# Performance work log

Measured on AMD Instinct MI355X. Metric: run time of the kernel, lower is better.

## Reference

```python
import jax, jax.numpy as jnp
import numpy as np

HEADS, DIM_HEAD = 8, 64
EPS = 1e-5  # torch InstanceNorm1d default


def instance_norm(t):
    # torch InstanceNorm1d(dim_head) applied to (b*h, n, d) normalizes over the
    # last dim d for each (b, h, n); affine=False, biased variance.
    mu = jnp.mean(t, axis=-1, keepdims=True)
    var = jnp.mean((t - mu) ** 2, axis=-1, keepdims=True)
    return (t - mu) * jax.lax.rsqrt(var + EPS)


def setup_inputs() -> dict:
    key = jax.random.key(0)
    k1, k2, k3, k4 = jax.random.split(key, 4)
    B, N, D = 8, 8192, 256
    inner = HEADS * DIM_HEAD  # 512
    x = jax.random.normal(k1, (B, N, D), jnp.float32)
    w_qkv = jax.random.normal(k2, (3 * inner, D), jnp.float32) / np.sqrt(D).astype(np.float32)
    w_out = jax.random.normal(k3, (D, inner), jnp.float32) / np.sqrt(inner).astype(np.float32)
    b_out = 0.01 * jax.random.normal(k4, (D,), jnp.float32)
    return {"x": x, "w_qkv": w_qkv, "w_out": w_out, "b_out": b_out}


def reference(x, w_qkv, w_out, b_out):
    B, N, _ = x.shape
    H, Dh = HEADS, DIM_HEAD
    # fused qkv projection: [B,N,3*H*Dh]
    qkv = jnp.einsum('bnd,ed->bne', x, w_qkv)
    q, k, v = jnp.split(qkv, 3, axis=-1)

    def to_heads(t):
        return t.reshape(B, N, H, Dh).transpose(0, 2, 1, 3)  # b h n d

    q, k, v = to_heads(q), to_heads(k), to_heads(v)
    # galerkin: instance-norm K and V
    k = instance_norm(k)
    v = instance_norm(v)
    # linear (non-softmax) attention: (K^T V) then Q @ (K^T V), scaled by 1/N
    dots = jnp.einsum('bhnd,bhne->bhde', k, v)            # [B,H,Dh,Dh]
    out = jnp.einsum('bhnd,bhde->bhne', q, dots) / N      # [B,H,N,Dh]
    out = out.transpose(0, 2, 1, 3).reshape(B, N, H * Dh)
    return jnp.einsum('bne,de->bnd', out, w_out) + b_out
```

## Files before the change

kernel.cpp:

```cpp
#include <hip/hip_runtime.h>
#include <hip/hip_bf16.h>
#include <stdint.h>

typedef __attribute__((ext_vector_type(8))) __bf16 bf16x8;
typedef __attribute__((ext_vector_type(8))) unsigned short ushort8_t;
typedef __attribute__((ext_vector_type(4))) unsigned short ushort4_t;
typedef __attribute__((ext_vector_type(4))) float f32x4;

#define MFMA16(a, b, c) __builtin_amdgcn_mfma_f32_16x16x32_bf16((a), (b), (c), 0, 0, 0)

static __device__ __forceinline__ unsigned short f2bf(float f) {
  union { float f; unsigned u; } v; v.f = f;
  unsigned r = v.u + 0x7fffu + ((v.u >> 16) & 1u);
  return (unsigned short)(r >> 16);
}
static __device__ __forceinline__ float bf2f(unsigned short u) {
  union { unsigned u; float f; } v; v.u = ((unsigned)u) << 16; return v.f;
}

static __device__ __forceinline__ void gld_lds16(const void* g, void* l) {
  __builtin_amdgcn_global_load_lds((const __attribute__((address_space(1))) void*)g,
                                   (__attribute__((address_space(3))) void*)l, 16, 0, 0);
}

__global__ __launch_bounds__(256) void k_conv(const float* __restrict__ x,
                                              const float* __restrict__ wqkv,
                                              const float* __restrict__ wout,
                                              unsigned short* __restrict__ xb,
                                              unsigned short* __restrict__ wqb,
                                              unsigned short* __restrict__ woutb) {
  const size_t NX = 4194304;
  const size_t NW = 98304;
  const size_t NO = 32768;
  const size_t stride = (size_t)gridDim.x * 256;
  for (size_t i4 = (size_t)blockIdx.x * 256 + threadIdx.x; i4 < NX + NW + NO; i4 += stride) {
    const float* src; unsigned short* dst; size_t off;
    if (i4 < NX)           { src = x;    dst = xb;    off = i4; }
    else if (i4 < NX + NW) { src = wqkv; dst = wqb;   off = i4 - NX; }
    else                   { src = wout; dst = woutb; off = i4 - NX - NW; }
    float4 v = ((const float4*)src)[off];
    ushort4_t o = { f2bf(v.x), f2bf(v.y), f2bf(v.z), f2bf(v.w) };
    *(ushort4_t*)(dst + off * 4) = o;
  }
}

__global__ __launch_bounds__(512) void k_fused(const unsigned short* __restrict__ xb,
                                               const unsigned short* __restrict__ wqb,
                                               float* __restrict__ partials) {
  __shared__ __align__(16) char smem[65536];
  unsigned short* As = (unsigned short*)smem;
  unsigned short* Bs = (unsigned short*)(smem + 32768);
  unsigned short* kt = (unsigned short*)smem;
  unsigned short* vt = (unsigned short*)(smem + 18432);

  const int t = threadIdx.x;
  const int w = t >> 6, lane = t & 63, lr = lane & 15, lg = lane >> 4;
  const int wr = w >> 1, wc = w & 1;
  const int dblk = w >> 1, ep = w & 1;

  const int id = blockIdx.x;
  const int nid = (id & 7) * 128 + (id >> 3);
  const int mg = nid >> 3, h = nid & 7;

  const int srl = lane >> 3, sc = lane & 7;
  const int swz = (sc ^ srl) << 3;

  const unsigned short* bptr[2];
  int aoff[2];
#pragma unroll
  for (int i = 0; i < 2; ++i) {
    const int br = (w * 2 + i) * 8 + srl;
    const int grow = (br < 64) ? (512 + h * 64 + br) : (1024 + h * 64 + (br - 64));
    bptr[i] = wqb + (size_t)grow * 256 + swz;
    aoff[i] = br * 256 + swz;
  }

  f32x4 acc2[2] = {f32x4{0.f, 0.f, 0.f, 0.f}, f32x4{0.f, 0.f, 0.f, 0.f}};

  for (int mi = 0; mi < 4; ++mi) {
    const long m0 = ((long)mg * 4 + mi) * 128;
    const unsigned short* am = xb + (size_t)m0 * 256;

#pragma unroll
    for (int i = 0; i < 2; ++i) {
      gld_lds16(am + aoff[i], &As[(w * 2 + i) * 512]);
      gld_lds16(bptr[i],      &Bs[(w * 2 + i) * 512]);
    }
    __syncthreads();

    f32x4 acc[2][4];
#pragma unroll
    for (int mb = 0; mb < 2; ++mb)
#pragma unroll
      for (int nb = 0; nb < 4; ++nb) acc[mb][nb] = f32x4{0.f, 0.f, 0.f, 0.f};

    for (int ktt = 0; ktt < 4; ++ktt) {
      const int cur = ktt & 1, nxt = cur ^ 1;
      if (ktt < 3) {
        const int k0 = (ktt + 1) * 64;
#pragma unroll
        for (int i = 0; i < 2; ++i) {
          gld_lds16(am + aoff[i] + k0, &As[nxt * 8192 + (w * 2 + i) * 512]);
          gld_lds16(bptr[i] + k0,      &Bs[nxt * 8192 + (w * 2 + i) * 512]);
        }
      }
      bf16x8 a[2][2], b[4][2];
#pragma unroll
      for (int mb = 0; mb < 2; ++mb) {
        const int R = wr * 32 + mb * 16 + lr;
#pragma unroll
        for (int kh = 0; kh < 2; ++kh)
          a[mb][kh] = *(const bf16x8*)&As[cur * 8192 + R * 64 + ((((kh << 2) + lg) ^ (R & 7)) << 3)];
      }
#pragma unroll
      for (int nb = 0; nb < 4; ++nb) {
        const int E = wc * 64 + nb * 16 + lr;
#pragma unroll
        for (int kh = 0; kh < 2; ++kh)
          b[nb][kh] = *(const bf16x8*)&Bs[cur * 8192 + E * 64 + ((((kh << 2) + lg) ^ (E & 7)) << 3)];
      }
#pragma unroll
      for (int mb = 0; mb < 2; ++mb)
#pragma unroll
        for (int nb = 0; nb < 4; ++nb)
#pragma unroll
          for (int kh = 0; kh < 2; ++kh)
            acc[mb][nb] = MFMA16(a[mb][kh], b[nb][kh], acc[mb][nb]);
      __syncthreads();
    }

    unsigned short* dst = (wc == 0) ? kt : vt;
#pragma unroll
    for (int mb = 0; mb < 2; ++mb) {
#pragma unroll
      for (int rg = 0; rg < 4; ++rg) {
        float s1 = acc[mb][0][rg] + acc[mb][1][rg] + acc[mb][2][rg] + acc[mb][3][rg];
        float s2 = acc[mb][0][rg] * acc[mb][0][rg] + acc[mb][1][rg] * acc[mb][1][rg] +
                   acc[mb][2][rg] * acc[mb][2][rg] + acc[mb][3][rg] * acc[mb][3][rg];
        s1 += __shfl_xor(s1, 1); s2 += __shfl_xor(s2, 1);
        s1 += __shfl_xor(s1, 2); s2 += __shfl_xor(s2, 2);
        s1 += __shfl_xor(s1, 4); s2 += __shfl_xor(s2, 4);
        s1 += __shfl_xor(s1, 8); s2 += __shfl_xor(s2, 8);
        const float mean = s1 * (1.f / 64.f);
        const float rs = rsqrtf(s2 * (1.f / 64.f) - mean * mean + 1e-5f);
        const int n = wr * 32 + mb * 16 + lg * 4 + rg;
        const int cn = n >> 6, nn = n & 63;
#pragma unroll
        for (int nb = 0; nb < 4; ++nb)
          dst[cn * 4608 + (nb * 16 + lr) * 72 + nn] = f2bf((acc[mb][nb][rg] - mean) * rs);
      }
    }
    __syncthreads();

#pragma unroll
    for (int cn = 0; cn < 2; ++cn) {
#pragma unroll
      for (int ns = 0; ns < 64; ns += 32) {
        bf16x8 af = *(const bf16x8*)&kt[cn * 4608 + (dblk * 16 + lr) * 72 + ns + lg * 8];
#pragma unroll
        for (int e = 0; e < 2; ++e) {
          bf16x8 bv = *(const bf16x8*)&vt[cn * 4608 + ((ep * 2 + e) * 16 + lr) * 72 + ns + lg * 8];
          acc2[e] = MFMA16(af, bv, acc2[e]);
        }
      }
    }
    __syncthreads();
  }

  float* pb = partials + ((size_t)mg * 8 + h) * 4096;
#pragma unroll
  for (int e = 0; e < 2; ++e)
#pragma unroll
    for (int rg = 0; rg < 4; ++rg) {
      const int d = dblk * 16 + lg * 4 + rg;
      const int eo = (ep * 2 + e) * 16 + lr;
      pb[d * 64 + eo] = acc2[e][rg];
    }
}

__global__ __launch_bounds__(256) void k_mmat(const float* __restrict__ partials,
                                              const float* __restrict__ wqkv,
                                              unsigned short* __restrict__ tmpT) {
  __shared__ float dl[4096];
  __shared__ float wqls[64 * 256];
  const int bh = blockIdx.x, b = bh >> 3, h = bh & 7;
  const int t = threadIdx.x;
#pragma unroll
  for (int i = 0; i < 4; ++i) {
    int off = t * 16 + i * 4;
    f32x4 s = {0.f, 0.f, 0.f, 0.f};
    for (int c = 0; c < 16; ++c) {
      const size_t chunk = (size_t)(b * 16 + c) * 8 + h;
      f32x4 p = *(const f32x4*)(partials + chunk * 4096 + off);
      s += p;
    }
    *(f32x4*)&dl[off] = s;
  }
#pragma unroll
  for (int i = 0; i < 16; ++i) {
    int idx4 = i * 256 + t;
    int d = idx4 >> 6, c4 = idx4 & 63;
    *(f32x4*)&wqls[d * 256 + c4 * 4] =
        *(const f32x4*)(wqkv + (size_t)(h * 64 + d) * 256 + c4 * 4);
  }
  __syncthreads();
  const int k = t;
  const float scale = 1.0f / 8192.0f;
  float res[64];
  for (int e = 0; e < 64; ++e) {
    float s = 0.f;
#pragma unroll
    for (int d = 0; d < 64; ++d) s += dl[d * 64 + e] * wqls[d * 256 + k];
    res[e] = s * scale;
  }
  unsigned short* dstp = tmpT + (size_t)b * 131072 + (size_t)k * 512 + h * 64;
#pragma unroll
  for (int e8 = 0; e8 < 8; ++e8) {
    ushort8_t o;
#pragma unroll
    for (int j = 0; j < 8; ++j) o[j] = f2bf(res[e8 * 8 + j]);
    *(ushort8_t*)(dstp + e8 * 8) = o;
  }
}

__global__ __launch_bounds__(256) void k_pmat(const unsigned short* __restrict__ woutb,
                                              const unsigned short* __restrict__ tmpT,
                                              unsigned short* __restrict__ pswz) {
  const int bid = blockIdx.x;
  const int b = bid >> 2, oq = (bid >> 1) & 1, kq = bid & 1;
  const int t = threadIdx.x, w = t >> 6, lane = t & 63, lr = lane & 15, lg = lane >> 4;
  const int wr = w >> 1, wc = w & 1;
  const int ob = oq * 128 + wr * 64, kb = kq * 128 + wc * 64;
  const unsigned short* tb = tmpT + (size_t)b * 131072;

  f32x4 acc[4][4];
#pragma unroll
  for (int mb = 0; mb < 4; ++mb)
#pragma unroll
    for (int nb = 0; nb < 4; ++nb) acc[mb][nb] = f32x4{0.f, 0.f, 0.f, 0.f};

  for (int ks = 0; ks < 16; ++ks) {
    bf16x8 a[4], bb[4];
#pragma unroll
    for (int mb = 0; mb < 4; ++mb)
      a[mb] = *(const bf16x8*)(woutb + (size_t)(ob + mb * 16 + lr) * 512 + ks * 32 + lg * 8);
#pragma unroll
    for (int nb = 0; nb < 4; ++nb)
      bb[nb] = *(const bf16x8*)(tb + (size_t)(kb + nb * 16 + lr) * 512 + ks * 32 + lg * 8);
#pragma unroll
    for (int mb = 0; mb < 4; ++mb)
#pragma unroll
      for (int nb = 0; nb < 4; ++nb) acc[mb][nb] = MFMA16(a[mb], bb[nb], acc[mb][nb]);
  }

  unsigned short* pb = pswz + (size_t)b * 65536;
#pragma unroll
  for (int mb = 0; mb < 4; ++mb)
#pragma unroll
    for (int nb = 0; nb < 4; ++nb)
#pragma unroll
      for (int rg = 0; rg < 4; ++rg) {
        int o = ob + mb * 16 + lg * 4 + rg;
        int k = kb + nb * 16 + lr;
        pb[(((k >> 5) * 16 + (o >> 4)) * 64 + (o & 15) + ((k >> 3) & 3) * 16) * 8 + (k & 7)] =
            f2bf(acc[mb][nb][rg]);
      }
}

__global__ __launch_bounds__(512) void k_gemm2(const unsigned short* __restrict__ xb,
                                               const unsigned short* __restrict__ pswz,
                                               const float* __restrict__ bout,
                                               float* __restrict__ out) {
  __shared__ __align__(16) char smem[65536];
  unsigned short* As = (unsigned short*)smem;
  float* lf = (float*)smem;

  const int b = blockIdx.x >> 6, mt = blockIdx.x & 63;
  const long m0 = (long)mt * 128;
  const int t = threadIdx.x, w = t >> 6, lane = t & 63, lr = lane & 15, lg = lane >> 4;
  const int wr = w >> 2, wc = w & 3;
  const unsigned short* qb = xb + ((size_t)b * 8192 + m0) * 256;
  const unsigned short* Mb = pswz + (size_t)b * 65536;
  const int srl = lane >> 3, sc = lane & 7;

#pragma unroll
  for (int i = 0; i < 2; ++i) {
    const int row = (i * 8 + w) * 8 + srl;
    gld_lds16(qb + (size_t)row * 256 + ((sc ^ (row & 7)) << 3),
              &As[(i * 8 + w) * 512]);
  }
  __syncthreads();

  f32x4 acc[4][4];
#pragma unroll
  for (int mb = 0; mb < 4; ++mb)
#pragma unroll
    for (int nb = 0; nb < 4; ++nb) acc[mb][nb] = f32x4{0.f, 0.f, 0.f, 0.f};

  for (int ks = 0; ks < 4; ++ks) {
    const int cur = ks & 1, nxt = cur ^ 1;
    if (ks < 3) {
      const int k0 = (ks + 1) * 64;
#pragma unroll
      for (int i = 0; i < 2; ++i) {
        const int row = (i * 8 + w) * 8 + srl;
        gld_lds16(qb + (size_t)row * 256 + k0 + ((sc ^ (row & 7)) << 3),
                  &As[nxt * 8192 + (i * 8 + w) * 512]);
      }
    }
    bf16x8 a[4][2], bfr[2][4];
#pragma unroll
    for (int mb = 0; mb < 4; ++mb) {
      const int R = wr * 64 + mb * 16 + lr;
#pragma unroll
      for (int kh = 0; kh < 2; ++kh)
        a[mb][kh] = *(const bf16x8*)&As[cur * 8192 + R * 64 + ((((kh << 2) + lg) ^ (R & 7)) << 3)];
    }
#pragma unroll
    for (int kh = 0; kh < 2; ++kh)
#pragma unroll
      for (int nb = 0; nb < 4; ++nb)
        bfr[kh][nb] = *(const bf16x8*)(Mb + ((((size_t)ks * 2 + kh) * 16 + wc * 4 + nb) * 64 + lane) * 8);
#pragma unroll
    for (int mb = 0; mb < 4; ++mb)
#pragma unroll
      for (int nb = 0; nb < 4; ++nb)
#pragma unroll
        for (int kh = 0; kh < 2; ++kh)
          acc[mb][nb] = MFMA16(a[mb][kh], bfr[kh][nb], acc[mb][nb]);
    __syncthreads();
  }

#pragma unroll
  for (int p = 0; p < 2; ++p) {
    if (wr == p) {
#pragma unroll
      for (int mb = 0; mb < 4; ++mb)
#pragma unroll
        for (int nb = 0; nb < 4; ++nb)
#pragma unroll
          for (int rg = 0; rg < 4; ++rg)
            lf[(mb * 16 + lg * 4 + rg) * 256 + wc * 64 + nb * 16 + lr] = acc[mb][nb][rg];
    }
    __syncthreads();
#pragma unroll
    for (int i = 0; i < 8; ++i) {
      const int idx = i * 512 + t;
      const int r = idx >> 6, c4 = idx & 63;
      f32x4 v = *(f32x4*)&lf[r * 256 + c4 * 4];
      f32x4 bo4 = *(const f32x4*)(bout + c4 * 4);
      v += bo4;
      *(f32x4*)(out + ((size_t)b * 8192 + m0 + p * 64 + r) * 256 + c4 * 4) = v;
    }
    __syncthreads();
  }
}

extern "C" void kernel_launch(void* const* d_in, const int* in_sizes, int n_in,
                              void* d_out, int out_size, void* d_ws, size_t ws_size,
                              hipStream_t stream) {
  const float* x    = (const float*)d_in[0];
  const float* wqkv = (const float*)d_in[1];
  const float* wout = (const float*)d_in[2];
  const float* bout = (const float*)d_in[3];
  float* out = (float*)d_out;

  char* ws = (char*)d_ws;
  unsigned short* xb = (unsigned short*)ws;
  size_t off = (size_t)65536 * 256 * 2;
  unsigned short* wqb = (unsigned short*)(ws + off);
  off += (size_t)1536 * 256 * 2;
  unsigned short* woutb = (unsigned short*)(ws + off);
  off += (size_t)256 * 512 * 2;
  float* partials = (float*)(ws + off);
  off += (size_t)1024 * 4096 * 4;
  unsigned short* tmpT = (unsigned short*)(ws + off);
  off += (size_t)8 * 131072 * 2;
  unsigned short* pswz = (unsigned short*)(ws + off);
  off += (size_t)8 * 65536 * 2;

  k_conv<<<4096, 256, 0, stream>>>(x, wqkv, wout, xb, wqb, woutb);
  k_fused<<<1024, 512, 0, stream>>>(xb, wqb, partials);
  k_mmat<<<64, 256, 0, stream>>>(partials, wqkv, tmpT);
  k_pmat<<<32, 256, 0, stream>>>(woutb, tmpT, pswz);
  k_gemm2<<<512, 512, 0, stream>>>(xb, pswz, bout, out);
}
```

Measured before the change: 164.4 us.

## Prefetch next M-tile during epilogue and relocate K/V scratch to avoid staging overlap

Moves the K/V normalized scratch buffers to the unused second halves of the A/B staging regions. This lets the first k-tile of the next M-tile be prefetched into buffer 0 during the last k-step and the normalization/KV-accumulation epilogue. Replaces some __syncthreads with LDS-only waitcnt plus barrier, drops the trailing barrier, switches the padded 72-stride scratch to an XOR-swizzled 64-stride layout, and fully unrolls the k loop. The goal is to hide global load latency across M-tiles, at the cost of subtler LDS hazard reasoning.

```diff
diff --git a/kernel.cpp b/kernel.cpp
--- a/kernel.cpp
+++ b/kernel.cpp
@@ -50,8 +50,8 @@
   __shared__ __align__(16) char smem[65536];
   unsigned short* As = (unsigned short*)smem;
   unsigned short* Bs = (unsigned short*)(smem + 32768);
-  unsigned short* kt = (unsigned short*)smem;
-  unsigned short* vt = (unsigned short*)(smem + 18432);
+  unsigned short* kt = (unsigned short*)smem + 8192;
+  unsigned short* vt = (unsigned short*)smem + 24576;
 
   const int t = threadIdx.x;
   const int w = t >> 6, lane = t & 63, lr = lane & 15, lg = lane >> 4;
@@ -77,15 +77,17 @@
 
   f32x4 acc2[2] = {f32x4{0.f, 0.f, 0.f, 0.f}, f32x4{0.f, 0.f, 0.f, 0.f}};
 
+  {
+    const unsigned short* am0 = xb + ((size_t)mg * 4 * 128) * 256;
+#pragma unroll
+    for (int i = 0; i < 2; ++i) {
+      gld_lds16(am0 + aoff[i], &As[(w * 2 + i) * 512]);
+      gld_lds16(bptr[i],       &Bs[(w * 2 + i) * 512]);
+    }
+  }
+
   for (int mi = 0; mi < 4; ++mi) {
-    const long m0 = ((long)mg * 4 + mi) * 128;
-    const unsigned short* am = xb + (size_t)m0 * 256;
-
-#pragma unroll
-    for (int i = 0; i < 2; ++i) {
-      gld_lds16(am + aoff[i], &As[(w * 2 + i) * 512]);
-      gld_lds16(bptr[i],      &Bs[(w * 2 + i) * 512]);
-    }
+    const unsigned short* am = xb + ((size_t)(mg * 4 + mi) * 128) * 256;
     __syncthreads();
 
     f32x4 acc[2][4];
@@ -94,6 +96,7 @@
 #pragma unroll
       for (int nb = 0; nb < 4; ++nb) acc[mb][nb] = f32x4{0.f, 0.f, 0.f, 0.f};
 
+#pragma unroll
     for (int ktt = 0; ktt < 4; ++ktt) {
       const int cur = ktt & 1, nxt = cur ^ 1;
       if (ktt < 3) {
@@ -103,6 +106,13 @@
           gld_lds16(am + aoff[i] + k0, &As[nxt * 8192 + (w * 2 + i) * 512]);
           gld_lds16(bptr[i] + k0,      &Bs[nxt * 8192 + (w * 2 + i) * 512]);
         }
+      } else if (mi < 3) {
+        const unsigned short* amn = am + 128 * 256;
+#pragma unroll
+        for (int i = 0; i < 2; ++i) {
+          gld_lds16(amn + aoff[i], &As[(w * 2 + i) * 512]);
+          gld_lds16(bptr[i],       &Bs[(w * 2 + i) * 512]);
+        }
       }
       bf16x8 a[2][2], b[4][2];
 #pragma unroll
@@ -126,7 +136,12 @@
 #pragma unroll
           for (int kh = 0; kh < 2; ++kh)
             acc[mb][nb] = MFMA16(a[mb][kh], b[nb][kh], acc[mb][nb]);
-      __syncthreads();
+      if (ktt < 3) {
+        __syncthreads();
+      } else {
+        asm volatile("s_waitcnt lgkmcnt(0)" ::: "memory");
+        __builtin_amdgcn_s_barrier();
+      }
     }
 
     unsigned short* dst = (wc == 0) ? kt : vt;
@@ -145,26 +160,33 @@
         const float rs = rsqrtf(s2 * (1.f / 64.f) - mean * mean + 1e-5f);
         const int n = wr * 32 + mb * 16 + lg * 4 + rg;
         const int cn = n >> 6, nn = n & 63;
-#pragma unroll
-        for (int nb = 0; nb < 4; ++nb)
-          dst[cn * 4608 + (nb * 16 + lr) * 72 + nn] = f2bf((acc[mb][nb][rg] - mean) * rs);
-      }
-    }
-    __syncthreads();
+        const int cc = nn >> 3, cj = nn & 7;
+#pragma unroll
+        for (int nb = 0; nb < 4; ++nb) {
+          const int d = nb * 16 + lr;
+          dst[cn * 4096 + d * 64 + ((cc ^ (d & 7)) << 3) + cj] =
+              f2bf((acc[mb][nb][rg] - mean) * rs);
+        }
+      }
+    }
+    asm volatile("s_waitcnt lgkmcnt(0)" ::: "memory");
+    __builtin_amdgcn_s_barrier();
 
 #pragma unroll
     for (int cn = 0; cn < 2; ++cn) {
 #pragma unroll
       for (int ns = 0; ns < 64; ns += 32) {
-        bf16x8 af = *(const bf16x8*)&kt[cn * 4608 + (dblk * 16 + lr) * 72 + ns + lg * 8];
+        const int cA = (ns >> 3) + lg;
+        const int dd = dblk * 16 + lr;
+        bf16x8 af = *(const bf16x8*)&kt[cn * 4096 + dd * 64 + ((cA ^ (dd & 7)) << 3)];
 #pragma unroll
         for (int e = 0; e < 2; ++e) {
-          bf16x8 bv = *(const bf16x8*)&vt[cn * 4608 + ((ep * 2 + e) * 16 + lr) * 72 + ns + lg * 8];
+          const int ee = (ep * 2 + e) * 16 + lr;
+          bf16x8 bv = *(const bf16x8*)&vt[cn * 4096 + ee * 64 + ((cA ^ (ee & 7)) << 3)];
           acc2[e] = MFMA16(af, bv, acc2[e]);
         }
       }
     }
-    __syncthreads();
   }
 
   float* pb = partials + ((size_t)mg * 8 + h) * 4096;
```

Result: slower. 172.2 us (+4.8%).

## Load QKV weight fragments directly from global and swizzle K/V LDS tiles

Applied to the files above, without the earlier changes.

The K/V projection's weight operand is no longer staged through LDS. Each wave reads its MFMA B fragments straight from global memory into registers, and the K-loop is fully unrolled. The normalized K/V tiles move to their own LDS region with an XOR-swizzled layout instead of a padded one. That separation lets the trailing barrier of each m-iteration be dropped. The cost is global or L2 latency inside the inner loop and repeated weight reads per wave in exchange for less LDS traffic and fewer barriers.

```diff
diff --git a/kernel.cpp b/kernel.cpp
--- a/kernel.cpp
+++ b/kernel.cpp
@@ -49,9 +49,8 @@
                                                float* __restrict__ partials) {
   __shared__ __align__(16) char smem[65536];
   unsigned short* As = (unsigned short*)smem;
-  unsigned short* Bs = (unsigned short*)(smem + 32768);
-  unsigned short* kt = (unsigned short*)smem;
-  unsigned short* vt = (unsigned short*)(smem + 18432);
+  unsigned short* kt = (unsigned short*)(smem + 32768);
+  unsigned short* vt = (unsigned short*)(smem + 49152);
 
   const int t = threadIdx.x;
   const int w = t >> 6, lane = t & 63, lr = lane & 15, lg = lane >> 4;
@@ -65,27 +64,22 @@
   const int srl = lane >> 3, sc = lane & 7;
   const int swz = (sc ^ srl) << 3;
 
-  const unsigned short* bptr[2];
   int aoff[2];
 #pragma unroll
-  for (int i = 0; i < 2; ++i) {
-    const int br = (w * 2 + i) * 8 + srl;
-    const int grow = (br < 64) ? (512 + h * 64 + br) : (1024 + h * 64 + (br - 64));
-    bptr[i] = wqb + (size_t)grow * 256 + swz;
-    aoff[i] = br * 256 + swz;
-  }
+  for (int i = 0; i < 2; ++i)
+    aoff[i] = ((w * 2 + i) * 8 + srl) * 256 + swz;
+
+  const int ebase = (wc == 0 ? 512 : 1024) + h * 64;
+  const unsigned short* bgp = wqb + (size_t)(ebase + lr) * 256 + lg * 8;
 
   f32x4 acc2[2] = {f32x4{0.f, 0.f, 0.f, 0.f}, f32x4{0.f, 0.f, 0.f, 0.f}};
 
   for (int mi = 0; mi < 4; ++mi) {
-    const long m0 = ((long)mg * 4 + mi) * 128;
-    const unsigned short* am = xb + (size_t)m0 * 256;
-
-#pragma unroll
-    for (int i = 0; i < 2; ++i) {
+    const unsigned short* am = xb + ((size_t)(mg * 4 + mi) * 128) * 256;
+
+#pragma unroll
+    for (int i = 0; i < 2; ++i)
       gld_lds16(am + aoff[i], &As[(w * 2 + i) * 512]);
-      gld_lds16(bptr[i],      &Bs[(w * 2 + i) * 512]);
-    }
     __syncthreads();
 
     f32x4 acc[2][4];
@@ -94,30 +88,28 @@
 #pragma unroll
       for (int nb = 0; nb < 4; ++nb) acc[mb][nb] = f32x4{0.f, 0.f, 0.f, 0.f};
 
+#pragma unroll
     for (int ktt = 0; ktt < 4; ++ktt) {
       const int cur = ktt & 1, nxt = cur ^ 1;
+      bf16x8 b[4][2];
+#pragma unroll
+      for (int nb = 0; nb < 4; ++nb)
+#pragma unroll
+        for (int kh = 0; kh < 2; ++kh)
+          b[nb][kh] = *(const bf16x8*)(bgp + (size_t)(nb * 16) * 256 + ktt * 64 + kh * 32);
       if (ktt < 3) {
         const int k0 = (ktt + 1) * 64;
 #pragma unroll
-        for (int i = 0; i < 2; ++i) {
+        for (int i = 0; i < 2; ++i)
           gld_lds16(am + aoff[i] + k0, &As[nxt * 8192 + (w * 2 + i) * 512]);
-          gld_lds16(bptr[i] + k0,      &Bs[nxt * 8192 + (w * 2 + i) * 512]);
-        }
-      }
-      bf16x8 a[2][2], b[4][2];
+      }
+      bf16x8 a[2][2];
 #pragma unroll
       for (int mb = 0; mb < 2; ++mb) {
         const int R = wr * 32 + mb * 16 + lr;
 #pragma unroll
         for (int kh = 0; kh < 2; ++kh)
           a[mb][kh] = *(const bf16x8*)&As[cur * 8192 + R * 64 + ((((kh << 2) + lg) ^ (R & 7)) << 3)];
-      }
-#pragma unroll
-      for (int nb = 0; nb < 4; ++nb) {
-        const int E = wc * 64 + nb * 16 + lr;
-#pragma unroll
-        for (int kh = 0; kh < 2; ++kh)
-          b[nb][kh] = *(const bf16x8*)&Bs[cur * 8192 + E * 64 + ((((kh << 2) + lg) ^ (E & 7)) << 3)];
       }
 #pragma unroll
       for (int mb = 0; mb < 2; ++mb)
@@ -145,9 +137,13 @@
         const float rs = rsqrtf(s2 * (1.f / 64.f) - mean * mean + 1e-5f);
         const int n = wr * 32 + mb * 16 + lg * 4 + rg;
         const int cn = n >> 6, nn = n & 63;
-#pragma unroll
-        for (int nb = 0; nb < 4; ++nb)
-          dst[cn * 4608 + (nb * 16 + lr) * 72 + nn] = f2bf((acc[mb][nb][rg] - mean) * rs);
+        const int cc = nn >> 3, cj = nn & 7;
+#pragma unroll
+        for (int nb = 0; nb < 4; ++nb) {
+          const int d = nb * 16 + lr;
+          dst[cn * 4096 + d * 64 + ((cc ^ (d & 7)) << 3) + cj] =
+              f2bf((acc[mb][nb][rg] - mean) * rs);
+        }
       }
     }
     __syncthreads();
@@ -156,15 +152,17 @@
     for (int cn = 0; cn < 2; ++cn) {
 #pragma unroll
       for (int ns = 0; ns < 64; ns += 32) {
-        bf16x8 af = *(const bf16x8*)&kt[cn * 4608 + (dblk * 16 + lr) * 72 + ns + lg * 8];
+        const int cA = (ns >> 3) + lg;
+        const int dd = dblk * 16 + lr;
+        bf16x8 af = *(const bf16x8*)&kt[cn * 4096 + dd * 64 + ((cA ^ (dd & 7)) << 3)];
 #pragma unroll
         for (int e = 0; e < 2; ++e) {
-          bf16x8 bv = *(const bf16x8*)&vt[cn * 4608 + ((ep * 2 + e) * 16 + lr) * 72 + ns + lg * 8];
+          const int ee = (ep * 2 + e) * 16 + lr;
+          bf16x8 bv = *(const bf16x8*)&vt[cn * 4096 + ee * 64 + ((cA ^ (ee & 7)) << 3)];
           acc2[e] = MFMA16(af, bv, acc2[e]);
         }
       }
     }
-    __syncthreads();
   }
 
   float* pb = partials + ((size_t)mg * 8 + h) * 4096;
```

After: 199.2 us. 21.2% more time.
